# Kernel optimization log

Measured on AMD Instinct MI355X. Metric: run time of the kernel, lower is better.

The kernel has to match this reference:

```python
import jax, jax.numpy as jnp
import numpy as np

B = 16384           # number of visits (segments)
EMB = 128           # embedding dim (hardcoded in module)
HID = 64            # hidden layer size
DIAG_LEN, PROC_LEN, MED_LEN = 2000, 1500, 153


def setup_inputs() -> dict:
    key = jax.random.key(0)
    ks = jax.random.split(key, 12)
    diag_codes = jax.random.randint(ks[0], (262144,), 0, DIAG_LEN)
    diag_seg = jnp.sort(jax.random.randint(ks[1], (262144,), 0, B))
    proc_codes = jax.random.randint(ks[2], (131072,), 0, PROC_LEN)
    proc_seg = jnp.sort(jax.random.randint(ks[3], (131072,), 0, B))
    med_codes = jax.random.randint(ks[4], (196608,), 0, MED_LEN)
    med_seg = jnp.sort(jax.random.randint(ks[5], (196608,), 0, B))
    diag_table = jax.random.normal(ks[6], (DIAG_LEN, EMB), dtype=jnp.float32)
    proc_table = jax.random.normal(ks[7], (PROC_LEN, EMB), dtype=jnp.float32)
    med_table = jax.random.normal(ks[8], (MED_LEN, EMB), dtype=jnp.float32)
    W1 = jax.random.normal(ks[9], (3 * EMB, HID), dtype=jnp.float32) * 0.05
    b1 = jnp.zeros((HID,), dtype=jnp.float32)
    W2 = jax.random.normal(ks[10], (HID, MED_LEN), dtype=jnp.float32) * 0.1
    b2 = jnp.zeros((MED_LEN,), dtype=jnp.float32)
    return {
        "diag_codes": diag_codes, "diag_seg": diag_seg,
        "proc_codes": proc_codes, "proc_seg": proc_seg,
        "med_codes": med_codes, "med_seg": med_seg,
        "diag_table": diag_table, "proc_table": proc_table, "med_table": med_table,
        "W1": W1, "b1": b1, "W2": W2, "b2": b2,
    }


def _embed_sum(table, codes, seg):
    # gather [N, EMB] then segment-sum to [B, EMB] (== per-visit sum of embeddings)
    return jax.ops.segment_sum(table[codes], seg, num_segments=B)


def reference(diag_codes, diag_seg, proc_codes, proc_seg, med_codes, med_seg,
              diag_table, proc_table, med_table, W1, b1, W2, b2):
    e_diag = _embed_sum(diag_table, diag_codes, diag_seg)   # [B, 128]
    e_proc = _embed_sum(proc_table, proc_codes, proc_seg)   # [B, 128]
    e_med = _embed_sum(med_table, med_codes, med_seg)       # [B, 128]
    x = jnp.concatenate([e_diag, e_proc, e_med], axis=1)    # [B, 384]
    h = jax.nn.relu(x @ W1 + b1)                            # [B, 64]
    return jax.nn.sigmoid(h @ W2 + b2)                      # [B, med_len]
```

## Files before the change

### kernel.cpp

```cpp
#include <hip/hip_runtime.h>
#include <hip/hip_bf16.h>

#define NVIS 16384
#define EMB 128
#define HID 64
#define MED 153
#define K1 384
#define VPB 16
#define NTHR 512
#define NBLK (NVIS / VPB)
#define CAPT 1536

#define W2F_OFF  0u
#define OFFS_OFF 20480u
#define OFFS_STRIDE 16388
#define TW_OFF   (20480u + 196656u)
#define WS_NEED  (217136u + 467584u)

#define ROWS_D 2000
#define ROWS_P 1500
#define ROWS_M 153
#define TBASE_D 0
#define TBASE_P 2000
#define TBASE_M 3500

#define SRCH_BLKS 193
#define TWB_D 500
#define TWB_P 375
#define TWB_M 39
#define TWB_ALL (TWB_D + TWB_P + TWB_M)
#define NW2F 1280
#define PREP_BLKS (SRCH_BLKS + TWB_ALL + 5)

typedef float f32x4 __attribute__((ext_vector_type(4)));
typedef short s16x8 __attribute__((ext_vector_type(8)));
typedef unsigned int u32;
typedef unsigned int u32x4 __attribute__((ext_vector_type(4)));

__device__ __forceinline__ unsigned short f2bf(float f) {
  union { float f; unsigned u; } v; v.f = f;
  unsigned r = v.u + 0x7FFFu + ((v.u >> 16) & 1u);
  return (unsigned short)(r >> 16);
}

__device__ __forceinline__ void acc8m(u32x4 t, float m, float* A) {
  union { unsigned u; float f; } c;
  c.u = t[0] << 16;          A[0] = fmaf(m, c.f, A[0]);
  c.u = t[0] & 0xFFFF0000u;  A[1] = fmaf(m, c.f, A[1]);
  c.u = t[1] << 16;          A[2] = fmaf(m, c.f, A[2]);
  c.u = t[1] & 0xFFFF0000u;  A[3] = fmaf(m, c.f, A[3]);
  c.u = t[2] << 16;          A[4] = fmaf(m, c.f, A[4]);
  c.u = t[2] & 0xFFFF0000u;  A[5] = fmaf(m, c.f, A[5]);
  c.u = t[3] << 16;          A[6] = fmaf(m, c.f, A[6]);
  c.u = t[3] & 0xFFFF0000u;  A[7] = fmaf(m, c.f, A[7]);
}

__device__ __forceinline__ int lb_scalar(const int* __restrict__ a, int lo, int hi, int key) {
  while (lo < hi) {
    int mid = (lo + hi) >> 1;
    if (a[mid] < key) lo = mid + 1; else hi = mid;
  }
  return lo;
}

__device__ __forceinline__ int lb_fast_scalar(const int* __restrict__ a, int n, int key) {
  long long g = ((long long)key * (long long)n) >> 14;
  int L = (int)g - 3072, R = (int)g + 3072;
  if (L < 0) L = 0;
  if (R > n) R = n;
  const bool ok = (L == 0 || a[L - 1] < key) && (R == n || a[R] >= key);
  if (!ok) { L = 0; R = n; }
  return lb_scalar(a, L, R, key);
}

__device__ __forceinline__ int lb_wave(const int* __restrict__ a, int n, int key, int lane) {
  long long g = ((long long)key * (long long)n) >> 14;
  int L = (int)g - 3072, R = (int)g + 3072;
  if (L < 0) L = 0;
  if (R > n) R = n;
  const bool ok = (L == 0 || a[L - 1] < key) && (R == n || a[R] >= key);
  if (!ok) { L = 0; R = n; }
  int lo = L - 1, hi = R;
  while (hi - lo > 1) {
    const int width = hi - lo - 1;
    const int p = lo + 1 + (int)(((long long)width * lane) >> 6);
    const bool lt = a[p] < key;
    const unsigned long long m = __ballot(lt);
    const int t = m ? (63 - __builtin_clzll(m)) : -1;
    const int nlo = (t >= 0) ? lo + 1 + (int)(((long long)width * t) >> 6) : lo;
    const int nhi = (t < 63) ? lo + 1 + (int)(((long long)width * (t + 1)) >> 6) : hi;
    lo = nlo; hi = nhi;
  }
  return hi;
}

__global__ __launch_bounds__(256, 4) void prep_kernel(
    const int* __restrict__ diag_seg, const int* __restrict__ proc_seg,
    const int* __restrict__ med_seg,
    const float* __restrict__ dT, const float* __restrict__ pT, const float* __restrict__ mT,
    const float* __restrict__ W1, const float* __restrict__ W2,
    unsigned char* __restrict__ ws, int ND, int NP, int NM)
{
  __shared__ float w1L[128 * 64];
  const int blk = blockIdx.x;
  const int tid = threadIdx.x;

  if (blk < SRCH_BLKS) {
    const int t = blk * 256 + tid;
    if (t < 3 * 16385) {
      const int T = t / 16385, k = t - T * 16385;
      const int* seg = (T == 0) ? diag_seg : (T == 1) ? proc_seg : med_seg;
      const int n = (T == 0) ? ND : (T == 1) ? NP : NM;
      ((int*)(ws + OFFS_OFF))[T * OFFS_STRIDE + k] = lb_fast_scalar(seg, n, k);
    }
  } else if (blk < SRCH_BLKS + TWB_ALL) {
    const int blk2 = blk - SRCH_BLKS;
    const float* tbl; int rows, r0, koff, tBase;
    if (blk2 < TWB_D)                { tbl = dT; rows = ROWS_D; r0 = blk2 * 4;            koff = 0;   tBase = TBASE_D; }
    else if (blk2 < TWB_D + TWB_P)   { tbl = pT; rows = ROWS_P; r0 = (blk2 - TWB_D) * 4;  koff = 128; tBase = TBASE_P; }
    else                             { tbl = mT; rows = ROWS_M; r0 = (blk2 - TWB_D - TWB_P) * 4; koff = 256; tBase = TBASE_M; }
    for (int i = tid; i < 128 * 64 / 4; i += 256)
      *(f32x4*)&w1L[i * 4] = *(const f32x4*)&W1[(size_t)koff * HID + i * 4];
    __syncthreads();
    const int r = r0 + (tid >> 6);
    const int j = tid & 63;
    if (r < rows) {
      float acc = 0.f;
      #pragma unroll 8
      for (int k4 = 0; k4 < 32; ++k4) {
        const f32x4 t = *(const f32x4*)(tbl + (size_t)r * EMB + k4 * 4);
        acc += t[0] * w1L[(k4 * 4 + 0) * 64 + j] + t[1] * w1L[(k4 * 4 + 1) * 64 + j]
             + t[2] * w1L[(k4 * 4 + 2) * 64 + j] + t[3] * w1L[(k4 * 4 + 3) * 64 + j];
      }
      *(unsigned short*)(ws + TW_OFF + (size_t)(tBase + r) * 128 + j * 2) = f2bf(acc);
    }
  } else {
    const int t = (blk - SRCH_BLKS - TWB_ALL) * 256 + tid;
    if (t < NW2F) {
      const int lane = t & 63, tk = t >> 6;
      const int kh = tk & 1, tile = tk >> 1;
      const int n = tile * 16 + (lane & 15);
      const int k0 = kh * 32 + (lane >> 4) * 8;
      unsigned short e0[8];
      #pragma unroll
      for (int e = 0; e < 8; ++e)
        e0[e] = (n < MED) ? f2bf(W2[(size_t)(k0 + e) * MED + n]) : (unsigned short)0;
      u32x4 o;
      o[0] = (u32)e0[0] | ((u32)e0[1] << 16);
      o[1] = (u32)e0[2] | ((u32)e0[3] << 16);
      o[2] = (u32)e0[4] | ((u32)e0[5] << 16);
      o[3] = (u32)e0[6] | ((u32)e0[7] << 16);
      *(u32x4*)(ws + W2F_OFF + (size_t)t * 16) = o;
    }
  }
}

__global__ __launch_bounds__(NTHR, 8) void fused_ehr_v7(
    const int* __restrict__ diag_codes, const int* __restrict__ proc_codes,
    const int* __restrict__ med_codes,
    const float* __restrict__ b1, const float* __restrict__ b2,
    const unsigned char* __restrict__ ws,
    float* __restrict__ out)
{
  __shared__ __align__(16) unsigned short hs[VPB][HID + 8];
  __shared__ int offsL[3][17];
  __shared__ int csL[17];
  __shared__ int twoffL[CAPT];

  const int tid = threadIdx.x;
  const int l = tid & 63;
  const int wv = tid >> 6;
  const int b0 = blockIdx.x * VPB;
  const int* offsAll = (const int*)(ws + OFFS_OFF);

  if (tid < 51) {
    const int T = tid / 17, idx = tid - T * 17;
    offsL[T][idx] = offsAll[T * OFFS_STRIDE + b0 + idx];
  }
  __syncthreads();
  if (tid < 17) {
    csL[tid] = (offsL[0][tid] - offsL[0][0]) + (offsL[1][tid] - offsL[1][0])
             + (offsL[2][tid] - offsL[2][0]);
  }
  __syncthreads();

  const int total = csL[16];
  const bool stAll = (total <= CAPT);

  if (stAll) {
#define STAGE(T, CG, TBASE)                                                     \
    {                                                                           \
      const int sT = offsL[T][0], cnt = offsL[T][16] - sT;                      \
      for (int i = tid; i < cnt; i += NTHR) {                                   \
        const int key = sT + i;                                                 \
        int lo = 0, hi = 16;                                                    \
        _Pragma("unroll")                                                       \
        for (int it = 0; it < 4; ++it) {                                        \
          const int m = (lo + hi) >> 1;                                         \
          if (offsL[T][m] <= key) lo = m; else hi = m;                          \
        }                                                                       \
        const int within = key - offsL[T][lo];                                  \
        int prior = 0;                                                          \
        if (T >= 1) prior += offsL[0][lo + 1] - offsL[0][lo];                   \
        if (T == 2) prior += offsL[1][lo + 1] - offsL[1][lo];                   \
        twoffL[csL[lo] + prior + within] = (TBASE + CG[key]) << 7;              \
      }                                                                         \
    }
    STAGE(0, diag_codes, TBASE_D)
    STAGE(1, proc_codes, TBASE_P)
    STAGE(2, med_codes,  TBASE_M)
#undef STAGE
  }
  __syncthreads();

  const int half = tid >> 5;
  const int ln = tid & 31;
  const int oct = ln >> 3;
  const int sl = ln & 7;
  const unsigned char* twb = ws + TW_OFF;

  float A[8] = {0.f, 0.f, 0.f, 0.f, 0.f, 0.f, 0.f, 0.f};

  if (stAll) {
    const int s = csL[half], e = csL[half + 1];
    for (int jj = s; jj < e; jj += 16) {
      const int j0 = jj + oct, j1 = jj + 4 + oct, j2 = jj + 8 + oct, j3 = jj + 12 + oct;
      const int i0 = (j0 < e) ? j0 : (e - 1);
      const int i1 = (j1 < e) ? j1 : (e - 1);
      const int i2 = (j2 < e) ? j2 : (e - 1);
      const int i3 = (j3 < e) ? j3 : (e - 1);
      const u32x4 t0 = *(const u32x4*)(twb + twoffL[i0] + sl * 16);
      const u32x4 t1 = *(const u32x4*)(twb + twoffL[i1] + sl * 16);
      const u32x4 t2 = *(const u32x4*)(twb + twoffL[i2] + sl * 16);
      const u32x4 t3 = *(const u32x4*)(twb + twoffL[i3] + sl * 16);
      acc8m(t0, (j0 < e) ? 1.f : 0.f, A);
      acc8m(t1, (j1 < e) ? 1.f : 0.f, A);
      acc8m(t2, (j2 < e) ? 1.f : 0.f, A);
      acc8m(t3, (j3 < e) ? 1.f : 0.f, A);
    }
  } else {
#define GFB(T, CG, TBASE)                                                       \
    {                                                                           \
      const int s = offsL[T][half], e = offsL[T][half + 1];                     \
      for (int jj = s; jj < e; jj += 8) {                                       \
        const int j0 = jj + oct, j1 = jj + 4 + oct;                             \
        const int i0 = (j0 < e) ? j0 : (e - 1);                                 \
        const int i1 = (j1 < e) ? j1 : (e - 1);                                 \
        const int o0 = (TBASE + CG[i0]) << 7;                                   \
        const int o1 = (TBASE + CG[i1]) << 7;                                   \
        const u32x4 t0 = *(const u32x4*)(twb + o0 + sl * 16);                   \
        const u32x4 t1 = *(const u32x4*)(twb + o1 + sl * 16);                   \
        acc8m(t0, (j0 < e) ? 1.f : 0.f, A);                                     \
        acc8m(t1, (j1 < e) ? 1.f : 0.f, A);                                     \
      }                                                                         \
    }
    GFB(0, diag_codes, TBASE_D)
    GFB(1, proc_codes, TBASE_P)
    GFB(2, med_codes,  TBASE_M)
#undef GFB
  }

  #pragma unroll
  for (int d = 0; d < 8; ++d) {
    A[d] += __shfl_xor(A[d], 8);
    A[d] += __shfl_xor(A[d], 16);
  }
  if (ln < 8) {
    const f32x4 bb0 = *(const f32x4*)(b1 + sl * 8);
    const f32x4 bb1 = *(const f32x4*)(b1 + sl * 8 + 4);
    u32x4 o;
    o[0] = (u32)f2bf(fmaxf(A[0] + bb0[0], 0.f)) | ((u32)f2bf(fmaxf(A[1] + bb0[1], 0.f)) << 16);
    o[1] = (u32)f2bf(fmaxf(A[2] + bb0[2], 0.f)) | ((u32)f2bf(fmaxf(A[3] + bb0[3], 0.f)) << 16);
    o[2] = (u32)f2bf(fmaxf(A[4] + bb1[0], 0.f)) | ((u32)f2bf(fmaxf(A[5] + bb1[1], 0.f)) << 16);
    o[3] = (u32)f2bf(fmaxf(A[6] + bb1[2], 0.f)) | ((u32)f2bf(fmaxf(A[7] + bb1[3], 0.f)) << 16);
    *(u32x4*)&hs[half][sl * 8] = o;
  }
  __syncthreads();

  const int jloc = l & 15;
  const int kq = l >> 4;
  const s16x8* w2f = (const s16x8*)(ws + W2F_OFF);

  for (int t = wv; t < 10; t += 8) {
    const int n = t * 16 + jloc;
    const bool nok = (n < MED);
    const s16x8 bw0 = w2f[(t * 2 + 0) * 64 + l];
    const s16x8 bw1 = w2f[(t * 2 + 1) * 64 + l];
    f32x4 o0 = {0.f, 0.f, 0.f, 0.f};
    {
      const int ko = kq * 8;
      const s16x8 a00 = *(const s16x8*)&hs[jloc][ko];
      o0 = __builtin_amdgcn_mfma_f32_16x16x32_bf16(a00, bw0, o0, 0, 0, 0);
      const s16x8 a01 = *(const s16x8*)&hs[jloc][ko + 32];
      o0 = __builtin_amdgcn_mfma_f32_16x16x32_bf16(a01, bw1, o0, 0, 0, 0);
    }
    if (nok) {
      const float bias2 = b2[n];
      #pragma unroll
      for (int r = 0; r < 4; ++r) {
        const int row = kq * 4 + r;
        const float z0 = o0[r] + bias2;
        out[(size_t)(b0 + row) * MED + n] = 1.f / (1.f + __expf(-z0));
      }
    }
  }
}

#define CAPD 640
#define CAPP 384
#define CAPM 512
#define CAPT_FB (CAPD + CAPP + CAPM)

__global__ __launch_bounds__(NTHR, 8) void fused_ehr_fb(
    const int* __restrict__ diag_codes, const int* __restrict__ diag_seg,
    const int* __restrict__ proc_codes, const int* __restrict__ proc_seg,
    const int* __restrict__ med_codes,  const int* __restrict__ med_seg,
    const float* __restrict__ diag_table, const float* __restrict__ proc_table,
    const float* __restrict__ med_table,
    const float* __restrict__ W1, const float* __restrict__ b1,
    const float* __restrict__ W2, const float* __restrict__ b2,
    float* __restrict__ out, int ND, int NP, int NM)
{
  __shared__ __align__(16) unsigned short xs[VPB][K1 + 8];
  __shared__ __align__(16) unsigned short hs[VPB][HID + 8];
  __shared__ int offs[3][VPB + 1];
  __shared__ int codesL[CAPT_FB];

  const int tid = threadIdx.x;
  const int l = tid & 63;
  const int wv = tid >> 6;
  const int b0 = blockIdx.x * VPB;

  if (wv < 6) {
    const int T = wv >> 1, w = wv & 1;
    const int* seg = (T == 0) ? diag_seg : (T == 1) ? proc_seg : med_seg;
    const int n = (T == 0) ? ND : (T == 1) ? NP : NM;
    const int r = lb_wave(seg, n, b0 + (w ? VPB : 0), l);
    if (l == 0) offs[T][w ? VPB : 0] = r;
  }
  __syncthreads();

  const int sD = offs[0][0], cntD = offs[0][VPB] - sD;
  const int sP = offs[1][0], cntP = offs[1][VPB] - sP;
  const int sM = offs[2][0], cntM = offs[2][VPB] - sM;
  const bool stD = (cntD <= CAPD), stP = (cntP <= CAPP), stM = (cntM <= CAPM);

  if (tid < 3 * (VPB - 1)) {
    const int T = tid / (VPB - 1), idx = tid - T * (VPB - 1) + 1;
    offs[T][idx] = offs[T][VPB];
  }
  if (stD) for (int i = tid; i < cntD; i += NTHR) codesL[i] = diag_codes[sD + i];
  if (stP) for (int i = tid; i < cntP; i += NTHR) codesL[CAPD + i] = proc_codes[sP + i];
  if (stM) for (int i = tid; i < cntM; i += NTHR) codesL[CAPD + CAPP + i] = med_codes[sM + i];
  __syncthreads();

#define MARK(Tidx, STAGED, CNT, SBASE, SEGG, NT)                                 \
  if (STAGED) {                                                                  \
    for (int i = tid; i < CNT; i += NTHR) {                                      \
      const int v1 = SEGG[SBASE + i];                                            \
      const int v0_ = (i == 0) ? (b0 - 1) : SEGG[SBASE + i - 1];                 \
      int klo = v0_ + 1; if (klo < b0 + 1) klo = b0 + 1;                         \
      int khi = v1;      if (khi > b0 + VPB - 1) khi = b0 + VPB - 1;             \
      for (int k = klo; k <= khi; ++k) offs[Tidx][k - b0] = SBASE + i;           \
    }                                                                            \
  } else if (tid < VPB - 1) {                                                    \
    offs[Tidx][tid + 1] = lb_fast_scalar(SEGG, NT, b0 + tid + 1);                \
  }

  MARK(0, stD, cntD, sD, diag_seg, ND)
  MARK(1, stP, cntP, sP, proc_seg, NP)
  MARK(2, stM, cntM, sM, med_seg,  NM)
#undef MARK
  __syncthreads();

  const int half = tid >> 5;
  const int ln = tid & 31;

#define GATH(T, CODES_G, TBL, STAGED, SGLOB, LBASE)                               \
  {                                                                               \
    const int s_ = offs[T][half], e_ = offs[T][half + 1];                         \
    float a0 = 0.f, a1 = 0.f, a2 = 0.f, a3 = 0.f;                                 \
    int i = s_;                                                                   \
    if (STAGED) {                                                                 \
      const int lb = LBASE - SGLOB;                                               \
      for (; i + 3 < e_; i += 4) {                                                \
        const int c0 = codesL[lb + i],     c1 = codesL[lb + i + 1];               \
        const int c2 = codesL[lb + i + 2], c3 = codesL[lb + i + 3];               \
        const f32x4 t0 = *(const f32x4*)(TBL + (size_t)c0 * EMB + ln * 4);        \
        const f32x4 t1 = *(const f32x4*)(TBL + (size_t)c1 * EMB + ln * 4);        \
        const f32x4 t2 = *(const f32x4*)(TBL + (size_t)c2 * EMB + ln * 4);        \
        const f32x4 t3 = *(const f32x4*)(TBL + (size_t)c3 * EMB + ln * 4);        \
        a0 += (t0[0] + t1[0]) + (t2[0] + t3[0]);                                  \
        a1 += (t0[1] + t1[1]) + (t2[1] + t3[1]);                                  \
        a2 += (t0[2] + t1[2]) + (t2[2] + t3[2]);                                  \
        a3 += (t0[3] + t1[3]) + (t2[3] + t3[3]);                                  \
      }                                                                           \
      for (; i < e_; ++i) {                                                       \
        const int c = codesL[lb + i];                                             \
        const f32x4 t = *(const f32x4*)(TBL + (size_t)c * EMB + ln * 4);          \
        a0 += t[0]; a1 += t[1]; a2 += t[2]; a3 += t[3];                           \
      }                                                                           \
    } else {                                                                      \
      for (; i < e_; ++i) {                                                       \
        const int c = CODES_G[i];                                                 \
        const f32x4 t = *(const f32x4*)(TBL + (size_t)c * EMB + ln * 4);          \
        a0 += t[0]; a1 += t[1]; a2 += t[2]; a3 += t[3];                           \
      }                                                                           \
    }                                                                             \
    const u32 p0 = (u32)f2bf(a0) | ((u32)f2bf(a1) << 16);                         \
    const u32 p1 = (u32)f2bf(a2) | ((u32)f2bf(a3) << 16);                         \
    uint2* d_ = (uint2*)&xs[half][T * EMB + ln * 4];                              \
    *d_ = make_uint2(p0, p1);                                                     \
  }

  GATH(0, diag_codes, diag_table, stD, sD, 0)
  GATH(1, proc_codes, proc_table, stP, sP, CAPD)
  GATH(2, med_codes,  med_table,  stM, sM, CAPD + CAPP)
#undef GATH
  __syncthreads();

  const int jloc = l & 15;
  const int kq = l >> 4;

  if (wv < 4) {
    const int j1 = wv * 16 + jloc;
    f32x4 acc = {0.f, 0.f, 0.f, 0.f};
    s16x8 bf;
    #pragma unroll
    for (int e = 0; e < 8; ++e)
      bf[e] = (short)f2bf(W1[(size_t)(kq * 8 + e) * HID + j1]);
    #pragma unroll
    for (int kt = 0; kt < 12; ++kt) {
      s16x8 nxt;
      if (kt < 11) {
        const int kb = (kt + 1) * 32 + kq * 8;
        #pragma unroll
        for (int e = 0; e < 8; ++e)
          nxt[e] = (short)f2bf(W1[(size_t)(kb + e) * HID + j1]);
      }
      const s16x8 a0 = *(const s16x8*)&xs[jloc][kt * 32 + kq * 8];
      acc = __builtin_amdgcn_mfma_f32_16x16x32_bf16(a0, bf, acc, 0, 0, 0);
      if (kt < 11) bf = nxt;
    }
    const float bias1 = b1[j1];
    #pragma unroll
    for (int r = 0; r < 4; ++r)
      hs[kq * 4 + r][j1] = f2bf(fmaxf(acc[r] + bias1, 0.f));
  }
  __syncthreads();

  for (int t = wv; t < 10; t += 8) {
    const int n = t * 16 + jloc;
    const bool nok = (n < MED);
    s16x8 bw0, bw1;
    #pragma unroll
    for (int e = 0; e < 8; ++e) {
      const int k0 = kq * 8 + e;
      bw0[e] = nok ? (short)f2bf(W2[(size_t)k0 * MED + n])        : (short)0;
      bw1[e] = nok ? (short)f2bf(W2[(size_t)(k0 + 32) * MED + n]) : (short)0;
    }
    f32x4 o0 = {0.f, 0.f, 0.f, 0.f};
    {
      const int ko = kq * 8;
      const s16x8 a00 = *(const s16x8*)&hs[jloc][ko];
      o0 = __builtin_amdgcn_mfma_f32_16x16x32_bf16(a00, bw0, o0, 0, 0, 0);
      const s16x8 a01 = *(const s16x8*)&hs[jloc][ko + 32];
      o0 = __builtin_amdgcn_mfma_f32_16x16x32_bf16(a01, bw1, o0, 0, 0, 0);
    }
    if (nok) {
      const float bias2 = b2[n];
      #pragma unroll
      for (int r = 0; r < 4; ++r) {
        const int row = kq * 4 + r;
        const float z0 = o0[r] + bias2;
        out[(size_t)(b0 + row) * MED + n] = 1.f / (1.f + __expf(-z0));
      }
    }
  }
}

extern "C" void kernel_launch(void* const* d_in, const int* in_sizes, int n_in,
                              void* d_out, int out_size, void* d_ws, size_t ws_size,
                              hipStream_t stream) {
  const int* diag_codes = (const int*)d_in[0];
  const int* diag_seg   = (const int*)d_in[1];
  const int* proc_codes = (const int*)d_in[2];
  const int* proc_seg   = (const int*)d_in[3];
  const int* med_codes  = (const int*)d_in[4];
  const int* med_seg    = (const int*)d_in[5];
  const float* diag_table = (const float*)d_in[6];
  const float* proc_table = (const float*)d_in[7];
  const float* med_table  = (const float*)d_in[8];
  const float* W1 = (const float*)d_in[9];
  const float* b1 = (const float*)d_in[10];
  const float* W2 = (const float*)d_in[11];
  const float* b2 = (const float*)d_in[12];
  float* out = (float*)d_out;

  if (ws_size >= WS_NEED) {
    unsigned char* ws = (unsigned char*)d_ws;
    prep_kernel<<<dim3(PREP_BLKS), dim3(256), 0, stream>>>(
        diag_seg, proc_seg, med_seg,
        diag_table, proc_table, med_table, W1, W2, ws,
        in_sizes[0], in_sizes[2], in_sizes[4]);
    fused_ehr_v7<<<dim3(NBLK), dim3(NTHR), 0, stream>>>(
        diag_codes, proc_codes, med_codes, b1, b2, ws, out);
  } else {
    fused_ehr_fb<<<dim3(NBLK), dim3(NTHR), 0, stream>>>(
        diag_codes, diag_seg, proc_codes, proc_seg, med_codes, med_seg,
        diag_table, proc_table, med_table, W1, b1, W2, b2, out,
        in_sizes[0], in_sizes[2], in_sizes[4]);
  }
}
```

Before: 25.56 us.

## Build segment offsets by scatter and serve med rows from shared memory

The prep kernel now builds segment offsets by having each element thread scatter its index across the gap between neighbouring segment ids, instead of running a binary search per visit. The main kernel copies the small 153-row projected med table into padded LDS once per block. Med codes are staged separately and accumulated from LDS, while diag and proc keep the global gather path. This cuts global gathers for med rows but adds a per-block LDS fill of about 20 KB and more launched prep blocks, which may lower occupancy.

```diff
diff --git a/kernel.cpp b/kernel.cpp
--- a/kernel.cpp
+++ b/kernel.cpp
@@ -9,7 +9,6 @@
 #define VPB 16
 #define NTHR 512
 #define NBLK (NVIS / VPB)
-#define CAPT 1536
 
 #define W2F_OFF  0u
 #define OFFS_OFF 20480u
@@ -24,13 +23,15 @@
 #define TBASE_P 2000
 #define TBASE_M 3500
 
-#define SRCH_BLKS 193
 #define TWB_D 500
 #define TWB_P 375
 #define TWB_M 39
 #define TWB_ALL (TWB_D + TWB_P + TWB_M)
 #define NW2F 1280
-#define PREP_BLKS (SRCH_BLKS + TWB_ALL + 5)
+
+#define CAP_DP 1024
+#define CAP_M  512
+#define MSTRIDE 144
 
 typedef float f32x4 __attribute__((ext_vector_type(4)));
 typedef short s16x8 __attribute__((ext_vector_type(8)));
@@ -104,17 +105,23 @@
   __shared__ float w1L[128 * 64];
   const int blk = blockIdx.x;
   const int tid = threadIdx.x;
-
-  if (blk < SRCH_BLKS) {
+  const int totSlots = ND + NP + NM + 3;
+  const int SB = (totSlots + 255) >> 8;
+
+  if (blk < SB) {
     const int t = blk * 256 + tid;
-    if (t < 3 * 16385) {
-      const int T = t / 16385, k = t - T * 16385;
-      const int* seg = (T == 0) ? diag_seg : (T == 1) ? proc_seg : med_seg;
-      const int n = (T == 0) ? ND : (T == 1) ? NP : NM;
-      ((int*)(ws + OFFS_OFF))[T * OFFS_STRIDE + k] = lb_fast_scalar(seg, n, k);
-    }
-  } else if (blk < SRCH_BLKS + TWB_ALL) {
-    const int blk2 = blk - SRCH_BLKS;
+    if (t < totSlots) {
+      int T, i, n; const int* seg;
+      if (t < ND + 1)               { T = 0; i = t;              n = ND; seg = diag_seg; }
+      else if (t < ND + NP + 2)     { T = 1; i = t - (ND + 1);   n = NP; seg = proc_seg; }
+      else                          { T = 2; i = t - (ND + NP + 2); n = NM; seg = med_seg; }
+      const int prev = (i == 0) ? -1 : seg[i - 1];
+      const int cur  = (i == n) ? NVIS : seg[i];
+      int* o = (int*)(ws + OFFS_OFF) + T * OFFS_STRIDE;
+      for (int k = prev + 1; k <= cur; ++k) o[k] = i;
+    }
+  } else if (blk < SB + TWB_ALL) {
+    const int blk2 = blk - SB;
     const float* tbl; int rows, r0, koff, tBase;
     if (blk2 < TWB_D)                { tbl = dT; rows = ROWS_D; r0 = blk2 * 4;            koff = 0;   tBase = TBASE_D; }
     else if (blk2 < TWB_D + TWB_P)   { tbl = pT; rows = ROWS_P; r0 = (blk2 - TWB_D) * 4;  koff = 128; tBase = TBASE_P; }
@@ -135,7 +142,7 @@
       *(unsigned short*)(ws + TW_OFF + (size_t)(tBase + r) * 128 + j * 2) = f2bf(acc);
     }
   } else {
-    const int t = (blk - SRCH_BLKS - TWB_ALL) * 256 + tid;
+    const int t = (blk - SB - TWB_ALL) * 256 + tid;
     if (t < NW2F) {
       const int lane = t & 63, tk = t >> 6;
       const int kh = tk & 1, tile = tk >> 1;
@@ -155,7 +162,7 @@
   }
 }
 
-__global__ __launch_bounds__(NTHR, 8) void fused_ehr_v7(
+__global__ __launch_bounds__(NTHR, 8) void fused_ehr_v8(
     const int* __restrict__ diag_codes, const int* __restrict__ proc_codes,
     const int* __restrict__ med_codes,
     const float* __restrict__ b1, const float* __restrict__ b2,
@@ -163,9 +170,11 @@
     float* __restrict__ out)
 {
   __shared__ __align__(16) unsigned short hs[VPB][HID + 8];
+  __shared__ __align__(16) unsigned char medTW[ROWS_M * MSTRIDE];
   __shared__ int offsL[3][17];
   __shared__ int csL[17];
-  __shared__ int twoffL[CAPT];
+  __shared__ int twoffL[CAP_DP];
+  __shared__ int medL[CAP_M];
 
   const int tid = threadIdx.x;
   const int l = tid & 63;
@@ -173,21 +182,30 @@
   const int b0 = blockIdx.x * VPB;
   const int* offsAll = (const int*)(ws + OFFS_OFF);
 
+  {
+    const unsigned char* src = ws + TW_OFF + (size_t)TBASE_M * 128;
+    for (int ch = tid; ch < (ROWS_M * 128) / 16; ch += NTHR) {
+      const u32x4 v = *(const u32x4*)(src + ch * 16);
+      const int row = ch >> 3, col = ch & 7;
+      *(u32x4*)&medTW[row * MSTRIDE + col * 16] = v;
+    }
+  }
   if (tid < 51) {
     const int T = tid / 17, idx = tid - T * 17;
     offsL[T][idx] = offsAll[T * OFFS_STRIDE + b0 + idx];
   }
   __syncthreads();
-  if (tid < 17) {
-    csL[tid] = (offsL[0][tid] - offsL[0][0]) + (offsL[1][tid] - offsL[1][0])
-             + (offsL[2][tid] - offsL[2][0]);
-  }
-  __syncthreads();
-
-  const int total = csL[16];
-  const bool stAll = (total <= CAPT);
-
-  if (stAll) {
+  if (tid < 17)
+    csL[tid] = (offsL[0][tid] - offsL[0][0]) + (offsL[1][tid] - offsL[1][0]);
+  __syncthreads();
+
+  const int totDP = csL[16];
+  const bool stDP = (totDP <= CAP_DP);
+  const int sMg = offsL[2][0];
+  const int cntM = offsL[2][16] - sMg;
+  const bool stM = (cntM <= CAP_M);
+
+  if (stDP) {
 #define STAGE(T, CG, TBASE)                                                     \
     {                                                                           \
       const int sT = offsL[T][0], cnt = offsL[T][16] - sT;                      \
@@ -201,16 +219,15 @@
         }                                                                       \
         const int within = key - offsL[T][lo];                                  \
         int prior = 0;                                                          \
-        if (T >= 1) prior += offsL[0][lo + 1] - offsL[0][lo];                   \
-        if (T == 2) prior += offsL[1][lo + 1] - offsL[1][lo];                   \
+        if (T == 1) prior = offsL[0][lo + 1] - offsL[0][lo];                    \
         twoffL[csL[lo] + prior + within] = (TBASE + CG[key]) << 7;              \
       }                                                                         \
     }
     STAGE(0, diag_codes, TBASE_D)
     STAGE(1, proc_codes, TBASE_P)
-    STAGE(2, med_codes,  TBASE_M)
 #undef STAGE
   }
+  if (stM) for (int i = tid; i < cntM; i += NTHR) medL[i] = med_codes[sMg + i];
   __syncthreads();
 
   const int half = tid >> 5;
@@ -221,7 +238,7 @@
 
   float A[8] = {0.f, 0.f, 0.f, 0.f, 0.f, 0.f, 0.f, 0.f};
 
-  if (stAll) {
+  if (stDP) {
     const int s = csL[half], e = csL[half + 1];
     for (int jj = s; jj < e; jj += 16) {
       const int j0 = jj + oct, j1 = jj + 4 + oct, j2 = jj + 8 + oct, j3 = jj + 12 + oct;
@@ -256,8 +273,30 @@
     }
     GFB(0, diag_codes, TBASE_D)
     GFB(1, proc_codes, TBASE_P)
-    GFB(2, med_codes,  TBASE_M)
 #undef GFB
+  }
+
+  {
+    const int s = offsL[2][half] - sMg, e = offsL[2][half + 1] - sMg;
+    for (int jj = s; jj < e; jj += 16) {
+      const int j0 = jj + oct, j1 = jj + 4 + oct, j2 = jj + 8 + oct, j3 = jj + 12 + oct;
+      const int i0 = (j0 < e) ? j0 : (e - 1);
+      const int i1 = (j1 < e) ? j1 : (e - 1);
+      const int i2 = (j2 < e) ? j2 : (e - 1);
+      const int i3 = (j3 < e) ? j3 : (e - 1);
+      const int c0 = stM ? medL[i0] : med_codes[sMg + i0];
+      const int c1 = stM ? medL[i1] : med_codes[sMg + i1];
+      const int c2 = stM ? medL[i2] : med_codes[sMg + i2];
+      const int c3 = stM ? medL[i3] : med_codes[sMg + i3];
+      const u32x4 t0 = *(const u32x4*)&medTW[c0 * MSTRIDE + sl * 16];
+      const u32x4 t1 = *(const u32x4*)&medTW[c1 * MSTRIDE + sl * 16];
+      const u32x4 t2 = *(const u32x4*)&medTW[c2 * MSTRIDE + sl * 16];
+      const u32x4 t3 = *(const u32x4*)&medTW[c3 * MSTRIDE + sl * 16];
+      acc8m(t0, (j0 < e) ? 1.f : 0.f, A);
+      acc8m(t1, (j1 < e) ? 1.f : 0.f, A);
+      acc8m(t2, (j2 < e) ? 1.f : 0.f, A);
+      acc8m(t3, (j3 < e) ? 1.f : 0.f, A);
+    }
   }
 
   #pragma unroll
@@ -499,11 +538,13 @@
 
   if (ws_size >= WS_NEED) {
     unsigned char* ws = (unsigned char*)d_ws;
-    prep_kernel<<<dim3(PREP_BLKS), dim3(256), 0, stream>>>(
+    const int totSlots = in_sizes[0] + in_sizes[2] + in_sizes[4] + 3;
+    const int SB = (totSlots + 255) >> 8;
+    prep_kernel<<<dim3(SB + TWB_ALL + 5), dim3(256), 0, stream>>>(
         diag_seg, proc_seg, med_seg,
         diag_table, proc_table, med_table, W1, W2, ws,
         in_sizes[0], in_sizes[2], in_sizes[4]);
-    fused_ehr_v7<<<dim3(NBLK), dim3(NTHR), 0, stream>>>(
+    fused_ehr_v8<<<dim3(NBLK), dim3(NTHR), 0, stream>>>(
         diag_codes, proc_codes, med_codes, b1, b2, ws, out);
   } else {
     fused_ehr_fb<<<dim3(NBLK), dim3(NTHR), 0, stream>>>(
```

Result: slower. 26.15 us (+2.3%).

## Split gather into LDS-resident hidden-slice kernel and separate MFMA output kernel

Applied to the files above, without the earlier changes.

The fused per-visit kernel is replaced by two kernels. A gather kernel holds one 8-wide hidden slice of the full projected table (all 3653 rows) in LDS, so each code lookup reads LDS instead of global memory. It writes the hidden activations to workspace, and a separate MFMA kernel computes the sigmoid output. Segment offsets are now built by a scatter over segment boundaries instead of per-visit binary searches. In exchange, every code index is re-read once per hidden slice (8 times), the workspace gains an extra round trip for the hidden activations, and there is one more launch.

```diff
diff --git a/kernel.cpp b/kernel.cpp
--- a/kernel.cpp
+++ b/kernel.cpp
@@ -6,31 +6,28 @@
 #define HID 64
 #define MED 153
 #define K1 384
-#define VPB 16
-#define NTHR 512
-#define NBLK (NVIS / VPB)
-#define CAPT 1536
+
+#define ROWS_D 2000
+#define ROWS_P 1500
+#define ROWS_M 153
+#define RT 3653
+#define TBASE_D 0
+#define TBASE_P 2000
+#define TBASE_M 3500
+#define E8S (RT * 16)
 
 #define W2F_OFF  0u
 #define OFFS_OFF 20480u
 #define OFFS_STRIDE 16388
-#define TW_OFF   (20480u + 196656u)
-#define WS_NEED  (217136u + 467584u)
-
-#define ROWS_D 2000
-#define ROWS_P 1500
-#define ROWS_M 153
-#define TBASE_D 0
-#define TBASE_P 2000
-#define TBASE_M 3500
-
-#define SRCH_BLKS 193
+#define TW_OFF   217136u
+#define H_OFF    684720u
+#define WS_NEED  (684720u + 2097152u)
+
 #define TWB_D 500
 #define TWB_P 375
 #define TWB_M 39
 #define TWB_ALL (TWB_D + TWB_P + TWB_M)
 #define NW2F 1280
-#define PREP_BLKS (SRCH_BLKS + TWB_ALL + 5)
 
 typedef float f32x4 __attribute__((ext_vector_type(4)));
 typedef short s16x8 __attribute__((ext_vector_type(8)));
@@ -104,21 +101,27 @@
   __shared__ float w1L[128 * 64];
   const int blk = blockIdx.x;
   const int tid = threadIdx.x;
-
-  if (blk < SRCH_BLKS) {
+  const int totSlots = ND + NP + NM + 3;
+  const int SB = (totSlots + 255) >> 8;
+
+  if (blk < SB) {
     const int t = blk * 256 + tid;
-    if (t < 3 * 16385) {
-      const int T = t / 16385, k = t - T * 16385;
-      const int* seg = (T == 0) ? diag_seg : (T == 1) ? proc_seg : med_seg;
-      const int n = (T == 0) ? ND : (T == 1) ? NP : NM;
-      ((int*)(ws + OFFS_OFF))[T * OFFS_STRIDE + k] = lb_fast_scalar(seg, n, k);
-    }
-  } else if (blk < SRCH_BLKS + TWB_ALL) {
-    const int blk2 = blk - SRCH_BLKS;
+    if (t < totSlots) {
+      int T, i, n; const int* seg;
+      if (t < ND + 1)           { T = 0; i = t;                 n = ND; seg = diag_seg; }
+      else if (t < ND + NP + 2) { T = 1; i = t - (ND + 1);      n = NP; seg = proc_seg; }
+      else                      { T = 2; i = t - (ND + NP + 2); n = NM; seg = med_seg; }
+      const int prev = (i == 0) ? -1 : seg[i - 1];
+      const int cur  = (i == n) ? NVIS : seg[i];
+      int* o = (int*)(ws + OFFS_OFF) + T * OFFS_STRIDE;
+      for (int k = prev + 1; k <= cur; ++k) o[k] = i;
+    }
+  } else if (blk < SB + TWB_ALL) {
+    const int blk2 = blk - SB;
     const float* tbl; int rows, r0, koff, tBase;
-    if (blk2 < TWB_D)                { tbl = dT; rows = ROWS_D; r0 = blk2 * 4;            koff = 0;   tBase = TBASE_D; }
-    else if (blk2 < TWB_D + TWB_P)   { tbl = pT; rows = ROWS_P; r0 = (blk2 - TWB_D) * 4;  koff = 128; tBase = TBASE_P; }
-    else                             { tbl = mT; rows = ROWS_M; r0 = (blk2 - TWB_D - TWB_P) * 4; koff = 256; tBase = TBASE_M; }
+    if (blk2 < TWB_D)              { tbl = dT; rows = ROWS_D; r0 = blk2 * 4;           koff = 0;   tBase = TBASE_D; }
+    else if (blk2 < TWB_D + TWB_P) { tbl = pT; rows = ROWS_P; r0 = (blk2 - TWB_D) * 4; koff = 128; tBase = TBASE_P; }
+    else                           { tbl = mT; rows = ROWS_M; r0 = (blk2 - TWB_D - TWB_P) * 4; koff = 256; tBase = TBASE_M; }
     for (int i = tid; i < 128 * 64 / 4; i += 256)
       *(f32x4*)&w1L[i * 4] = *(const f32x4*)&W1[(size_t)koff * HID + i * 4];
     __syncthreads();
@@ -132,10 +135,11 @@
         acc += t[0] * w1L[(k4 * 4 + 0) * 64 + j] + t[1] * w1L[(k4 * 4 + 1) * 64 + j]
              + t[2] * w1L[(k4 * 4 + 2) * 64 + j] + t[3] * w1L[(k4 * 4 + 3) * 64 + j];
       }
-      *(unsigned short*)(ws + TW_OFF + (size_t)(tBase + r) * 128 + j * 2) = f2bf(acc);
+      *(unsigned short*)(ws + TW_OFF + (size_t)(j >> 3) * E8S
+                         + (size_t)(tBase + r) * 16 + (size_t)(j & 7) * 2) = f2bf(acc);
     }
   } else {
-    const int t = (blk - SRCH_BLKS - TWB_ALL) * 256 + tid;
+    const int t = (blk - SB - TWB_ALL) * 256 + tid;
     if (t < NW2F) {
       const int lane = t & 63, tk = t >> 6;
       const int kh = tk & 1, tile = tk >> 1;
@@ -155,157 +159,109 @@
   }
 }
 
-__global__ __launch_bounds__(NTHR, 8) void fused_ehr_v7(
+__global__ __launch_bounds__(1024, 8) void gather8_kernel(
     const int* __restrict__ diag_codes, const int* __restrict__ proc_codes,
     const int* __restrict__ med_codes,
-    const float* __restrict__ b1, const float* __restrict__ b2,
-    const unsigned char* __restrict__ ws,
-    float* __restrict__ out)
+    const float* __restrict__ b1,
+    unsigned char* __restrict__ ws)
 {
-  __shared__ __align__(16) unsigned short hs[VPB][HID + 8];
-  __shared__ int offsL[3][17];
-  __shared__ int csL[17];
-  __shared__ int twoffL[CAPT];
+  __shared__ __align__(16) u32x4 twL[RT];
+  __shared__ int offsB[3][257];
 
   const int tid = threadIdx.x;
-  const int l = tid & 63;
-  const int wv = tid >> 6;
-  const int b0 = blockIdx.x * VPB;
+  const int e8 = blockIdx.x >> 6;
+  const int v0 = (blockIdx.x & 63) * 256;
+
+  const unsigned char* src = ws + TW_OFF + (size_t)e8 * E8S;
+  for (int k = tid; k < RT; k += 1024)
+    twL[k] = *(const u32x4*)(src + (size_t)k * 16);
   const int* offsAll = (const int*)(ws + OFFS_OFF);
-
-  if (tid < 51) {
-    const int T = tid / 17, idx = tid - T * 17;
-    offsL[T][idx] = offsAll[T * OFFS_STRIDE + b0 + idx];
-  }
-  __syncthreads();
-  if (tid < 17) {
-    csL[tid] = (offsL[0][tid] - offsL[0][0]) + (offsL[1][tid] - offsL[1][0])
-             + (offsL[2][tid] - offsL[2][0]);
-  }
-  __syncthreads();
-
-  const int total = csL[16];
-  const bool stAll = (total <= CAPT);
-
-  if (stAll) {
-#define STAGE(T, CG, TBASE)                                                     \
-    {                                                                           \
-      const int sT = offsL[T][0], cnt = offsL[T][16] - sT;                      \
-      for (int i = tid; i < cnt; i += NTHR) {                                   \
-        const int key = sT + i;                                                 \
-        int lo = 0, hi = 16;                                                    \
-        _Pragma("unroll")                                                       \
-        for (int it = 0; it < 4; ++it) {                                        \
-          const int m = (lo + hi) >> 1;                                         \
-          if (offsL[T][m] <= key) lo = m; else hi = m;                          \
-        }                                                                       \
-        const int within = key - offsL[T][lo];                                  \
-        int prior = 0;                                                          \
-        if (T >= 1) prior += offsL[0][lo + 1] - offsL[0][lo];                   \
-        if (T == 2) prior += offsL[1][lo + 1] - offsL[1][lo];                   \
-        twoffL[csL[lo] + prior + within] = (TBASE + CG[key]) << 7;              \
-      }                                                                         \
-    }
-    STAGE(0, diag_codes, TBASE_D)
-    STAGE(1, proc_codes, TBASE_P)
-    STAGE(2, med_codes,  TBASE_M)
-#undef STAGE
-  }
-  __syncthreads();
-
-  const int half = tid >> 5;
-  const int ln = tid & 31;
-  const int oct = ln >> 3;
-  const int sl = ln & 7;
-  const unsigned char* twb = ws + TW_OFF;
-
+  for (int t = tid; t < 3 * 257; t += 1024) {
+    const int T = (t < 257) ? 0 : (t < 514) ? 1 : 2;
+    const int idx = t - T * 257;
+    offsB[T][idx] = offsAll[T * OFFS_STRIDE + v0 + idx];
+  }
+  __syncthreads();
+
+  const int v = tid >> 2;
+  const int l4 = tid & 3;
   float A[8] = {0.f, 0.f, 0.f, 0.f, 0.f, 0.f, 0.f, 0.f};
 
-  if (stAll) {
-    const int s = csL[half], e = csL[half + 1];
-    for (int jj = s; jj < e; jj += 16) {
-      const int j0 = jj + oct, j1 = jj + 4 + oct, j2 = jj + 8 + oct, j3 = jj + 12 + oct;
-      const int i0 = (j0 < e) ? j0 : (e - 1);
-      const int i1 = (j1 < e) ? j1 : (e - 1);
-      const int i2 = (j2 < e) ? j2 : (e - 1);
-      const int i3 = (j3 < e) ? j3 : (e - 1);
-      const u32x4 t0 = *(const u32x4*)(twb + twoffL[i0] + sl * 16);
-      const u32x4 t1 = *(const u32x4*)(twb + twoffL[i1] + sl * 16);
-      const u32x4 t2 = *(const u32x4*)(twb + twoffL[i2] + sl * 16);
-      const u32x4 t3 = *(const u32x4*)(twb + twoffL[i3] + sl * 16);
-      acc8m(t0, (j0 < e) ? 1.f : 0.f, A);
-      acc8m(t1, (j1 < e) ? 1.f : 0.f, A);
-      acc8m(t2, (j2 < e) ? 1.f : 0.f, A);
-      acc8m(t3, (j3 < e) ? 1.f : 0.f, A);
-    }
-  } else {
-#define GFB(T, CG, TBASE)                                                       \
-    {                                                                           \
-      const int s = offsL[T][half], e = offsL[T][half + 1];                     \
-      for (int jj = s; jj < e; jj += 8) {                                       \
-        const int j0 = jj + oct, j1 = jj + 4 + oct;                             \
-        const int i0 = (j0 < e) ? j0 : (e - 1);                                 \
-        const int i1 = (j1 < e) ? j1 : (e - 1);                                 \
-        const int o0 = (TBASE + CG[i0]) << 7;                                   \
-        const int o1 = (TBASE + CG[i1]) << 7;                                   \
-        const u32x4 t0 = *(const u32x4*)(twb + o0 + sl * 16);                   \
-        const u32x4 t1 = *(const u32x4*)(twb + o1 + sl * 16);                   \
-        acc8m(t0, (j0 < e) ? 1.f : 0.f, A);                                     \
-        acc8m(t1, (j1 < e) ? 1.f : 0.f, A);                                     \
-      }                                                                         \
-    }
-    GFB(0, diag_codes, TBASE_D)
-    GFB(1, proc_codes, TBASE_P)
-    GFB(2, med_codes,  TBASE_M)
-#undef GFB
-  }
+#define G8(T, CG, TBASE)                                                    \
+  {                                                                         \
+    const int s = offsB[T][v], e = offsB[T][v + 1];                         \
+    for (int i = s + l4; i < e; i += 8) {                                   \
+      const int j1 = i + 4;                                                 \
+      const int i1 = (j1 < e) ? j1 : (e - 1);                               \
+      const int c0 = TBASE + CG[i];                                         \
+      const int c1 = TBASE + CG[i1];                                        \
+      const u32x4 t0 = twL[c0];                                             \
+      const u32x4 t1 = twL[c1];                                             \
+      acc8m(t0, 1.f, A);                                                    \
+      acc8m(t1, (j1 < e) ? 1.f : 0.f, A);                                   \
+    }                                                                       \
+  }
+  G8(0, diag_codes, TBASE_D)
+  G8(1, proc_codes, TBASE_P)
+  G8(2, med_codes,  TBASE_M)
+#undef G8
 
   #pragma unroll
   for (int d = 0; d < 8; ++d) {
-    A[d] += __shfl_xor(A[d], 8);
-    A[d] += __shfl_xor(A[d], 16);
-  }
-  if (ln < 8) {
-    const f32x4 bb0 = *(const f32x4*)(b1 + sl * 8);
-    const f32x4 bb1 = *(const f32x4*)(b1 + sl * 8 + 4);
+    A[d] += __shfl_xor(A[d], 1);
+    A[d] += __shfl_xor(A[d], 2);
+  }
+  if (l4 == 0) {
+    const f32x4 bb0 = *(const f32x4*)(b1 + e8 * 8);
+    const f32x4 bb1 = *(const f32x4*)(b1 + e8 * 8 + 4);
     u32x4 o;
     o[0] = (u32)f2bf(fmaxf(A[0] + bb0[0], 0.f)) | ((u32)f2bf(fmaxf(A[1] + bb0[1], 0.f)) << 16);
     o[1] = (u32)f2bf(fmaxf(A[2] + bb0[2], 0.f)) | ((u32)f2bf(fmaxf(A[3] + bb0[3], 0.f)) << 16);
     o[2] = (u32)f2bf(fmaxf(A[4] + bb1[0], 0.f)) | ((u32)f2bf(fmaxf(A[5] + bb1[1], 0.f)) << 16);
     o[3] = (u32)f2bf(fmaxf(A[6] + bb1[2], 0.f)) | ((u32)f2bf(fmaxf(A[7] + bb1[3], 0.f)) << 16);
-    *(u32x4*)&hs[half][sl * 8] = o;
-  }
-  __syncthreads();
-
+    *(u32x4*)(ws + H_OFF + (size_t)(v0 + v) * 128 + e8 * 16) = o;
+  }
+}
+
+__global__ __launch_bounds__(256, 8) void mlp2_kernel(
+    const unsigned char* __restrict__ ws,
+    const float* __restrict__ b2, float* __restrict__ out)
+{
+  const int tid = threadIdx.x;
+  const int l = tid & 63;
+  const int wv = tid >> 6;
   const int jloc = l & 15;
   const int kq = l >> 4;
+  const int m0 = blockIdx.x * 16;
+  const unsigned char* h = ws + H_OFF;
   const s16x8* w2f = (const s16x8*)(ws + W2F_OFF);
 
-  for (int t = wv; t < 10; t += 8) {
+  const s16x8 a00 = *(const s16x8*)(h + (size_t)(m0 + jloc) * 128 + kq * 16);
+  const s16x8 a01 = *(const s16x8*)(h + (size_t)(m0 + jloc) * 128 + 64 + kq * 16);
+
+  for (int t = wv; t < 10; t += 4) {
     const int n = t * 16 + jloc;
     const bool nok = (n < MED);
     const s16x8 bw0 = w2f[(t * 2 + 0) * 64 + l];
     const s16x8 bw1 = w2f[(t * 2 + 1) * 64 + l];
     f32x4 o0 = {0.f, 0.f, 0.f, 0.f};
-    {
-      const int ko = kq * 8;
-      const s16x8 a00 = *(const s16x8*)&hs[jloc][ko];
-      o0 = __builtin_amdgcn_mfma_f32_16x16x32_bf16(a00, bw0, o0, 0, 0, 0);
-      const s16x8 a01 = *(const s16x8*)&hs[jloc][ko + 32];
-      o0 = __builtin_amdgcn_mfma_f32_16x16x32_bf16(a01, bw1, o0, 0, 0, 0);
-    }
+    o0 = __builtin_amdgcn_mfma_f32_16x16x32_bf16(a00, bw0, o0, 0, 0, 0);
+    o0 = __builtin_amdgcn_mfma_f32_16x16x32_bf16(a01, bw1, o0, 0, 0, 0);
     if (nok) {
       const float bias2 = b2[n];
       #pragma unroll
       for (int r = 0; r < 4; ++r) {
         const int row = kq * 4 + r;
         const float z0 = o0[r] + bias2;
-        out[(size_t)(b0 + row) * MED + n] = 1.f / (1.f + __expf(-z0));
+        out[(size_t)(m0 + row) * MED + n] = 1.f / (1.f + __expf(-z0));
       }
     }
   }
 }
 
+#define VPB 16
+#define NTHR 512
+#define NBLK (NVIS / VPB)
 #define CAPD 640
 #define CAPP 384
 #define CAPM 512
@@ -497,14 +453,19 @@
   const float* b2 = (const float*)d_in[12];
   float* out = (float*)d_out;
 
-  if (ws_size >= WS_NEED) {
+  const bool sizes_ok = (in_sizes[6] == ROWS_D * EMB) && (in_sizes[7] == ROWS_P * EMB)
+                     && (in_sizes[8] == ROWS_M * EMB);
+  if (ws_size >= WS_NEED && sizes_ok) {
     unsigned char* ws = (unsigned char*)d_ws;
-    prep_kernel<<<dim3(PREP_BLKS), dim3(256), 0, stream>>>(
+    const int totSlots = in_sizes[0] + in_sizes[2] + in_sizes[4] + 3;
+    const int SB = (totSlots + 255) >> 8;
+    prep_kernel<<<dim3(SB + TWB_ALL + 5), dim3(256), 0, stream>>>(
         diag_seg, proc_seg, med_seg,
         diag_table, proc_table, med_table, W1, W2, ws,
         in_sizes[0], in_sizes[2], in_sizes[4]);
-    fused_ehr_v7<<<dim3(NBLK), dim3(NTHR), 0, stream>>>(
-        diag_codes, proc_codes, med_codes, b1, b2, ws, out);
+    gather8_kernel<<<dim3(512), dim3(1024), 0, stream>>>(
+        diag_codes, proc_codes, med_codes, b1, ws);
+    mlp2_kernel<<<dim3(NVIS / 16), dim3(256), 0, stream>>>(ws, b2, out);
   } else {
     fused_ehr_fb<<<dim3(NBLK), dim3(NTHR), 0, stream>>>(
         diag_codes, diag_seg, proc_codes, proc_seg, med_codes, med_seg,
```

After: 29.51 us. 15.5% more time.

## Build segment offsets by scatter-from-boundaries and batch table-projection rows per block

Applied to the files above, without the earlier changes.

Segment offset construction no longer binary-searches each of the 3x16385 visit boundaries. Each sorted segment element now compares itself with its predecessor and writes its index into every offset slot it starts, giving one coalesced pass over the segment arrays. The table-times-W1 projection blocks now handle 16 rows each instead of 4, so the W1 slice is loaded into shared memory a quarter as often. The prep grid is sized from the input lengths, which means launching many more small search blocks, and the fast path is guarded by a table-size check.

```diff
diff --git a/kernel.cpp b/kernel.cpp
--- a/kernel.cpp
+++ b/kernel.cpp
@@ -24,13 +24,11 @@
 #define TBASE_P 2000
 #define TBASE_M 3500
 
-#define SRCH_BLKS 193
-#define TWB_D 500
-#define TWB_P 375
-#define TWB_M 39
+#define TWB_D 125
+#define TWB_P 94
+#define TWB_M 10
 #define TWB_ALL (TWB_D + TWB_P + TWB_M)
 #define NW2F 1280
-#define PREP_BLKS (SRCH_BLKS + TWB_ALL + 5)
 
 typedef float f32x4 __attribute__((ext_vector_type(4)));
 typedef short s16x8 __attribute__((ext_vector_type(8)));
@@ -104,38 +102,47 @@
   __shared__ float w1L[128 * 64];
   const int blk = blockIdx.x;
   const int tid = threadIdx.x;
-
-  if (blk < SRCH_BLKS) {
+  const int totSlots = ND + NP + NM + 3;
+  const int SB = (totSlots + 255) >> 8;
+
+  if (blk < SB) {
     const int t = blk * 256 + tid;
-    if (t < 3 * 16385) {
-      const int T = t / 16385, k = t - T * 16385;
-      const int* seg = (T == 0) ? diag_seg : (T == 1) ? proc_seg : med_seg;
-      const int n = (T == 0) ? ND : (T == 1) ? NP : NM;
-      ((int*)(ws + OFFS_OFF))[T * OFFS_STRIDE + k] = lb_fast_scalar(seg, n, k);
-    }
-  } else if (blk < SRCH_BLKS + TWB_ALL) {
-    const int blk2 = blk - SRCH_BLKS;
+    if (t < totSlots) {
+      int T, i, n; const int* seg;
+      if (t < ND + 1)           { T = 0; i = t;                 n = ND; seg = diag_seg; }
+      else if (t < ND + NP + 2) { T = 1; i = t - (ND + 1);      n = NP; seg = proc_seg; }
+      else                      { T = 2; i = t - (ND + NP + 2); n = NM; seg = med_seg; }
+      const int prev = (i == 0) ? -1 : seg[i - 1];
+      const int cur  = (i == n) ? NVIS : seg[i];
+      int* o = (int*)(ws + OFFS_OFF) + T * OFFS_STRIDE;
+      for (int k = prev + 1; k <= cur; ++k) o[k] = i;
+    }
+  } else if (blk < SB + TWB_ALL) {
+    const int blk2 = blk - SB;
     const float* tbl; int rows, r0, koff, tBase;
-    if (blk2 < TWB_D)                { tbl = dT; rows = ROWS_D; r0 = blk2 * 4;            koff = 0;   tBase = TBASE_D; }
-    else if (blk2 < TWB_D + TWB_P)   { tbl = pT; rows = ROWS_P; r0 = (blk2 - TWB_D) * 4;  koff = 128; tBase = TBASE_P; }
-    else                             { tbl = mT; rows = ROWS_M; r0 = (blk2 - TWB_D - TWB_P) * 4; koff = 256; tBase = TBASE_M; }
+    if (blk2 < TWB_D)              { tbl = dT; rows = ROWS_D; r0 = blk2 * 16;           koff = 0;   tBase = TBASE_D; }
+    else if (blk2 < TWB_D + TWB_P) { tbl = pT; rows = ROWS_P; r0 = (blk2 - TWB_D) * 16; koff = 128; tBase = TBASE_P; }
+    else                           { tbl = mT; rows = ROWS_M; r0 = (blk2 - TWB_D - TWB_P) * 16; koff = 256; tBase = TBASE_M; }
     for (int i = tid; i < 128 * 64 / 4; i += 256)
       *(f32x4*)&w1L[i * 4] = *(const f32x4*)&W1[(size_t)koff * HID + i * 4];
     __syncthreads();
-    const int r = r0 + (tid >> 6);
     const int j = tid & 63;
-    if (r < rows) {
-      float acc = 0.f;
-      #pragma unroll 8
-      for (int k4 = 0; k4 < 32; ++k4) {
-        const f32x4 t = *(const f32x4*)(tbl + (size_t)r * EMB + k4 * 4);
-        acc += t[0] * w1L[(k4 * 4 + 0) * 64 + j] + t[1] * w1L[(k4 * 4 + 1) * 64 + j]
-             + t[2] * w1L[(k4 * 4 + 2) * 64 + j] + t[3] * w1L[(k4 * 4 + 3) * 64 + j];
+    #pragma unroll
+    for (int rr = 0; rr < 4; ++rr) {
+      const int r = r0 + rr * 4 + (tid >> 6);
+      if (r < rows) {
+        float acc = 0.f;
+        #pragma unroll 8
+        for (int k4 = 0; k4 < 32; ++k4) {
+          const f32x4 t = *(const f32x4*)(tbl + (size_t)r * EMB + k4 * 4);
+          acc += t[0] * w1L[(k4 * 4 + 0) * 64 + j] + t[1] * w1L[(k4 * 4 + 1) * 64 + j]
+               + t[2] * w1L[(k4 * 4 + 2) * 64 + j] + t[3] * w1L[(k4 * 4 + 3) * 64 + j];
+        }
+        *(unsigned short*)(ws + TW_OFF + (size_t)(tBase + r) * 128 + j * 2) = f2bf(acc);
       }
-      *(unsigned short*)(ws + TW_OFF + (size_t)(tBase + r) * 128 + j * 2) = f2bf(acc);
     }
   } else {
-    const int t = (blk - SRCH_BLKS - TWB_ALL) * 256 + tid;
+    const int t = (blk - SB - TWB_ALL) * 256 + tid;
     if (t < NW2F) {
       const int lane = t & 63, tk = t >> 6;
       const int kh = tk & 1, tile = tk >> 1;
@@ -155,7 +162,7 @@
   }
 }
 
-__global__ __launch_bounds__(NTHR, 8) void fused_ehr_v7(
+__global__ __launch_bounds__(NTHR, 8) void fused_ehr_v10(
     const int* __restrict__ diag_codes, const int* __restrict__ proc_codes,
     const int* __restrict__ med_codes,
     const float* __restrict__ b1, const float* __restrict__ b2,
@@ -497,13 +504,17 @@
   const float* b2 = (const float*)d_in[12];
   float* out = (float*)d_out;
 
-  if (ws_size >= WS_NEED) {
+  const bool sizes_ok = (in_sizes[6] == ROWS_D * EMB) && (in_sizes[7] == ROWS_P * EMB)
+                     && (in_sizes[8] == ROWS_M * EMB);
+  if (ws_size >= WS_NEED && sizes_ok) {
     unsigned char* ws = (unsigned char*)d_ws;
-    prep_kernel<<<dim3(PREP_BLKS), dim3(256), 0, stream>>>(
+    const int totSlots = in_sizes[0] + in_sizes[2] + in_sizes[4] + 3;
+    const int SB = (totSlots + 255) >> 8;
+    prep_kernel<<<dim3(SB + TWB_ALL + 5), dim3(256), 0, stream>>>(
         diag_seg, proc_seg, med_seg,
         diag_table, proc_table, med_table, W1, W2, ws,
         in_sizes[0], in_sizes[2], in_sizes[4]);
-    fused_ehr_v7<<<dim3(NBLK), dim3(NTHR), 0, stream>>>(
+    fused_ehr_v10<<<dim3(NBLK), dim3(NTHR), 0, stream>>>(
         diag_codes, proc_codes, med_codes, b1, b2, ws, out);
   } else {
     fused_ehr_fb<<<dim3(NBLK), dim3(NTHR), 0, stream>>>(
```

Result: slower. 32.05 us (+25.4%).
